# Optimization experiments

Hardware: AMD Instinct MI355X
Metric: run time of the kernel (lower is better)

## Reference

```python
import jax, jax.numpy as jnp
import numpy as np

H = 150  # hidden per direction

def _lstm_dir(x, w_ih, w_hh, b_ih, b_hh):
    # x: [B, T, D] -> hs: [B, T, H]; PyTorch gate order i,f,g,o
    B = x.shape[0]
    xg = jnp.einsum('btd,gd->btg', x, w_ih) + b_ih + b_hh  # precompute input projection [B,T,4H]
    def step(carry, xt):
        h, c = carry
        g = xt + h @ w_hh.T
        i, f, gg, o = jnp.split(g, 4, axis=-1)
        i, f, o = jax.nn.sigmoid(i), jax.nn.sigmoid(f), jax.nn.sigmoid(o)
        c = f * c + i * jnp.tanh(gg)
        h = o * jnp.tanh(c)
        return (h, c), h
    init = (jnp.zeros((B, H), x.dtype), jnp.zeros((B, H), x.dtype))
    _, hs = jax.lax.scan(step, init, jnp.swapaxes(xg, 0, 1))  # [T,B,H]
    return jnp.swapaxes(hs, 0, 1)

def _bilstm(x, w_ih_f, w_hh_f, b_ih_f, b_hh_f, w_ih_b, w_hh_b, b_ih_b, b_hh_b):
    fwd = _lstm_dir(x, w_ih_f, w_hh_f, b_ih_f, b_hh_f)
    bwd = jnp.flip(_lstm_dir(jnp.flip(x, axis=1), w_ih_b, w_hh_b, b_ih_b, b_hh_b), axis=1)
    return jnp.concatenate([fwd, bwd], axis=-1)  # [B, T, 2H]

def setup_inputs() -> dict:
    key = jax.random.key(0)
    ks = jax.random.split(key, 20)
    s = 0.05
    d = {
        'sentences': jax.random.normal(ks[0], (1024, 128, 343), jnp.float32),
        'w_ih_f1': jax.random.normal(ks[1], (600, 343)) * s,
        'w_hh_f1': jax.random.normal(ks[2], (600, 150)) * s,
        'b_ih_f1': jax.random.normal(ks[3], (600,)) * s,
        'b_hh_f1': jax.random.normal(ks[4], (600,)) * s,
        'w_ih_b1': jax.random.normal(ks[5], (600, 343)) * s,
        'w_hh_b1': jax.random.normal(ks[6], (600, 150)) * s,
        'b_ih_b1': jax.random.normal(ks[7], (600,)) * s,
        'b_hh_b1': jax.random.normal(ks[8], (600,)) * s,
        'w_ih_f2': jax.random.normal(ks[9], (600, 300)) * s,
        'w_hh_f2': jax.random.normal(ks[10], (600, 150)) * s,
        'b_ih_f2': jax.random.normal(ks[11], (600,)) * s,
        'b_hh_f2': jax.random.normal(ks[12], (600,)) * s,
        'w_ih_b2': jax.random.normal(ks[13], (600, 300)) * s,
        'w_hh_b2': jax.random.normal(ks[14], (600, 150)) * s,
        'b_ih_b2': jax.random.normal(ks[15], (600,)) * s,
        'b_hh_b2': jax.random.normal(ks[16], (600,)) * s,
        'w_out': jax.random.normal(ks[17], (7, 300)) * s,
        'b_out': jax.random.normal(ks[18], (7,)) * s,
    }
    return d

def reference(sentences, w_ih_f1, w_hh_f1, b_ih_f1, b_hh_f1, w_ih_b1, w_hh_b1, b_ih_b1, b_hh_b1,
              w_ih_f2, w_hh_f2, b_ih_f2, b_hh_f2, w_ih_b2, w_hh_b2, b_ih_b2, b_hh_b2, w_out, b_out):
    # Layer 1: per-sentence BiLSTM over words, batched instead of a python loop (dropout is eval-mode identity)
    word_out = _bilstm(sentences, w_ih_f1, w_hh_f1, b_ih_f1, b_hh_f1, w_ih_b1, w_hh_b1, b_ih_b1, b_hh_b1)  # [S,T,300]
    sent_emb = jnp.max(word_out, axis=1)  # max-pool over words -> [S,300]
    # Layer 2: BiLSTM over the sequence of sentence embeddings (batch of 1 paragraph)
    sent_out = _bilstm(sent_emb[None], w_ih_f2, w_hh_f2, b_ih_f2, b_hh_f2, w_ih_b2, w_hh_b2, b_ih_b2, b_hh_b2)[0]  # [S,300]
    log_probs = jax.nn.log_softmax(sent_out @ w_out.T + b_out, axis=-1)  # [S,7]
    return log_probs
```

## Files before the change

kernel.cpp:

```cpp
#include <hip/hip_runtime.h>
#include <hip/hip_bf16.h>
#include <hip/hip_fp16.h>

typedef short bf16x8 __attribute__((ext_vector_type(8)));
typedef float f32x4 __attribute__((ext_vector_type(4)));
typedef unsigned short u16x4 __attribute__((ext_vector_type(4)));
typedef unsigned int uint32;

#define MFMA_B16(a,b,c) __builtin_amdgcn_mfma_f32_16x16x32_bf16(a,b,c,0,0,0)

#define NS   1024
#define TLEN 128
#define DD   343
#define HH   150
#define GG   600
#define KX   352
#define XR   360
#define HR   168
#define KXP  44
#define NP   640
#define NG2  640

#define OFF_WXP  0u
#define OFF_WHP  901120u
#define OFF_B1   1310720u
#define OFF_W2B  1315840u
#define OFF_W2I  1725440u
#define OFF_SE   3184640u
#define OFF_XG2  4413440u
#define OFF_H2O  9656320u
#define OFF_XG1  10885120ull

#define PE0 450560
#define PE1 655360
#define PE2 656640
#define PE3 861440
#define PE4 1226240

__device__ __forceinline__ float rcp_fast(float x) { return __builtin_amdgcn_rcpf(x); }
__device__ __forceinline__ float sigm(float x) { return rcp_fast(1.f + __expf(-x)); }
__device__ __forceinline__ float tanh_fast(float x) { return 1.f - 2.f * rcp_fast(__expf(2.f * x) + 1.f); }

__device__ __forceinline__ void bar_lds() {
  asm volatile("s_waitcnt lgkmcnt(0)" ::: "memory");
  __builtin_amdgcn_s_barrier();
  asm volatile("" ::: "memory");
}

__device__ __forceinline__ unsigned short f2bu(float v) {
  __hip_bfloat16 b = __float2bfloat16(v);
  return __builtin_bit_cast(unsigned short, b);
}

__global__ __launch_bounds__(256) void prep_kernel(
    const float* __restrict__ wif1, const float* __restrict__ whf1,
    const float* __restrict__ bif1, const float* __restrict__ bhf1,
    const float* __restrict__ wib1, const float* __restrict__ whb1,
    const float* __restrict__ bib1, const float* __restrict__ bhb1,
    const float* __restrict__ wif2, const float* __restrict__ wib2,
    const float* __restrict__ whf2, const float* __restrict__ whb2,
    __hip_bfloat16* __restrict__ WXp, __hip_bfloat16* __restrict__ WHp,
    float* __restrict__ B1, __hip_bfloat16* __restrict__ W2B, float* __restrict__ W2I)
{
  int i = blockIdx.x * 256 + threadIdx.x;
  if (i < PE0) {
    int d = i / 225280; int r = i - d * 225280;
    int p = r / 5120;   int r2 = r - p * 5120;
    int n2 = r2 >> 3;   int jj = r2 & 7;
    int k = p * 8 + jj;
    int g = n2 / 160, j = n2 - g * 160;
    const float* w = d ? wib1 : wif1;
    float v = (j < HH && k < DD) ? w[(g * HH + j) * DD + k] : 0.f;
    WXp[i] = __float2bfloat16(v);
  } else if (i < PE1) {
    int ii = i - PE0;
    int d = ii / 102400; int r = ii - d * 102400;
    int p = r / 5120;    int r2 = r - p * 5120;
    int n2 = r2 >> 3;    int jj = r2 & 7;
    int k = p * 8 + jj;
    int g = n2 / 160, j = n2 - g * 160;
    const float* w = d ? whb1 : whf1;
    float v = (j < HH && k < HH) ? w[(g * HH + j) * HH + k] : 0.f;
    WHp[ii] = __float2bfloat16(v);
  } else if (i < PE2) {
    int ii = i - PE1;
    int d = ii / NP; int n2 = ii - d * NP;
    int g = n2 / 160, j = n2 - g * 160;
    float v = 0.f;
    if (j < HH) {
      int n = g * HH + j;
      v = d ? (bib1[n] + bhb1[n]) : (bif1[n] + bhf1[n]);
    }
    B1[ii] = v;
  } else if (i < PE3) {
    int ii = i - PE2;
    int d = ii / 102400; int r = ii - d * 102400;
    int n2 = r / 160;    int k = r - n2 * 160;
    int g = n2 / 160, j = n2 - g * 160;
    const float* w = d ? whb2 : whf2;
    float v = (j < HH && k < HH) ? w[(g * HH + j) * HH + k] : 0.f;
    W2B[ii] = __float2bfloat16(v);
  } else if (i < PE4) {
    int ii = i - PE3;
    int d = ii / 182400; int r = ii - d * 182400;
    int k = r / 608;     int n = r - k * 608;
    const float* w = d ? wib2 : wif2;
    float v = (n < GG) ? w[n * 300 + k] : 0.f;
    W2I[ii] = v;
  }
}

#define GA_SMEM (128u * 720u)

__global__ __launch_bounds__(512) void xg1_gemm(
    const float* __restrict__ x, const __hip_bfloat16* __restrict__ WXp,
    const float* __restrict__ B1, __hip_bfloat16* __restrict__ XG1,
    int sBase, int CS)
{
  extern __shared__ char smem[];
  __hip_bfloat16* xsA = (__hip_bfloat16*)smem;

  const int mtl = blockIdx.x;
  const int sg = sBase + mtl;

  const int tid = threadIdx.x;
  const int lane = tid & 63;
  const int wv = tid >> 6;
  const int wr = wv >> 2;
  const int wc = wv & 3;
  const int c16 = lane & 15;
  const int kgrp = lane >> 4;

  for (int g = tid; g < 11264; g += 512) {
    int row = g / 88;
    int c4 = (g - row * 88) * 4;
    const float* src = x + ((size_t)sg * TLEN + row) * DD + c4;
    float v0 = 0.f, v1 = 0.f, v2 = 0.f, v3 = 0.f;
    if (c4 + 3 < DD) { v0 = src[0]; v1 = src[1]; v2 = src[2]; v3 = src[3]; }
    else {
      if (c4 < DD)     v0 = src[0];
      if (c4 + 1 < DD) v1 = src[1];
      if (c4 + 2 < DD) v2 = src[2];
    }
    u16x4 o;
    o.x = f2bu(v0); o.y = f2bu(v1); o.z = f2bu(v2); o.w = f2bu(v3);
    *(u16x4*)(smem + row * 720 + c4 * 2) = o;
  }
  bar_lds();

  for (int dir = 0; dir < 2; ++dir) {
    const __hip_bfloat16* WXd = WXp + (size_t)dir * KXP * NP * 8;
    __hip_bfloat16* outd = XG1 + ((size_t)dir * CS + mtl) * TLEN * NG2;

    #pragma unroll
    for (int nh = 0; nh < 2; ++nh) {
      const int nbase = nh * 320 + wc * 80;
      f32x4 acc[4][5];
      #pragma unroll
      for (int mi = 0; mi < 4; ++mi)
        #pragma unroll
        for (int nf = 0; nf < 5; ++nf) acc[mi][nf] = (f32x4){0.f, 0.f, 0.f, 0.f};

      for (int kk = 0; kk < 11; ++kk) {
        bf16x8 a[4], b[5];
        #pragma unroll
        for (int mi = 0; mi < 4; ++mi)
          a[mi] = *reinterpret_cast<const bf16x8*>(
              xsA + (wr * 64 + mi * 16 + c16) * XR + kk * 32 + kgrp * 8);
        #pragma unroll
        for (int nf = 0; nf < 5; ++nf)
          b[nf] = *reinterpret_cast<const bf16x8*>(
              WXd + ((size_t)(kk * 4 + kgrp) * NP + nbase + nf * 16 + c16) * 8);
        #pragma unroll
        for (int mi = 0; mi < 4; ++mi)
          #pragma unroll
          for (int nf = 0; nf < 5; ++nf)
            acc[mi][nf] = MFMA_B16(a[mi], b[nf], acc[mi][nf]);
      }

      float bias[5];
      #pragma unroll
      for (int nf = 0; nf < 5; ++nf)
        bias[nf] = B1[dir * NP + nbase + nf * 16 + c16];

      #pragma unroll
      for (int mi = 0; mi < 4; ++mi)
        #pragma unroll
        for (int r = 0; r < 4; ++r) {
          int t = wr * 64 + mi * 16 + kgrp * 4 + r;
          __hip_bfloat16* row = outd + (size_t)t * NG2;
          #pragma unroll
          for (int nf = 0; nf < 5; ++nf)
            row[nbase + nf * 16 + c16] = __float2bfloat16(acc[mi][nf][r] + bias[nf]);
        }
    }
  }
}

__global__ __launch_bounds__(640) void lstm1_rec(
    const __hip_bfloat16* __restrict__ XG1, const __hip_bfloat16* __restrict__ WHp,
    float* __restrict__ SE, int sBase, int CS)
{
  __shared__ __hip_bfloat16 hs[16 * HR];

  const int tid = threadIdx.x;
  const int lane = tid & 63;
  const int wv = tid >> 6;
  const int dir = blockIdx.x & 1;
  const int grp = blockIdx.x >> 1;
  const int cls0 = grp * 8;
  const int s0g = sBase + cls0;
  const int c16 = lane & 15;
  const int kgrp = lane >> 4;
  const int j = wv * 16 + c16;

  for (int e = tid; e < 16 * HR; e += 640) hs[e] = __float2bfloat16(0.f);

  const __hip_bfloat16* WHd = WHp + (size_t)dir * 20 * NP * 8;
  bf16x8 whr[5][4];
  #pragma unroll
  for (int kh = 0; kh < 5; ++kh)
    #pragma unroll
    for (int g4 = 0; g4 < 4; ++g4) {
      whr[kh][g4] = *reinterpret_cast<const bf16x8*>(
          WHd + ((size_t)(kh * 4 + kgrp) * NP + g4 * 160 + j) * 8);
      asm volatile("" : "+v"(whr[kh][g4]));
    }

  float creg[4] = {0.f, 0.f, 0.f, 0.f};
  float mxr[4] = {-3e38f, -3e38f, -3e38f, -3e38f};

  const __hip_bfloat16* xgd = XG1 + (size_t)dir * CS * TLEN * NG2;
  const int sentb = cls0 + (kgrp & 1) * 4;
  const int par = kgrp >> 1;

  float xq[16], xqN[16];
  #pragma unroll
  for (int g4 = 0; g4 < 4; ++g4)
    #pragma unroll
    for (int r = 0; r < 4; ++r) {
      int tt = dir ? (127 - par) : par;
      xq[g4 * 4 + r] = __bfloat162float(
          xgd[((size_t)(sentb + r) * TLEN + tt) * NG2 + g4 * 160 + j]);
    }
  __syncthreads();

  for (int p = 0; p < 64; ++p) {
    f32x4 acc[4];
    #pragma unroll
    for (int g4 = 0; g4 < 4; ++g4) {
      acc[g4][0] = xq[g4 * 4 + 0]; acc[g4][1] = xq[g4 * 4 + 1];
      acc[g4][2] = xq[g4 * 4 + 2]; acc[g4][3] = xq[g4 * 4 + 3];
    }
    if (p < 63) {
      #pragma unroll
      for (int g4 = 0; g4 < 4; ++g4)
        #pragma unroll
        for (int r = 0; r < 4; ++r) {
          int tl = 2 * (p + 1) + par;
          int tt = dir ? (127 - tl) : tl;
          xqN[g4 * 4 + r] = __bfloat162float(
              xgd[((size_t)(sentb + r) * TLEN + tt) * NG2 + g4 * 160 + j]);
        }
    }
    #pragma unroll
    for (int kh = 0; kh < 5; ++kh) {
      bf16x8 ah = *reinterpret_cast<const bf16x8*>(hs + c16 * HR + kh * 32 + kgrp * 8);
      #pragma unroll
      for (int g4 = 0; g4 < 4; ++g4)
        acc[g4] = MFMA_B16(ah, whr[kh][g4], acc[g4]);
    }
    {
      const bool act = (kgrp < 2);
      #pragma unroll
      for (int r = 0; r < 4; ++r) {
        float iv = sigm(acc[0][r]);
        float fv = sigm(acc[1][r]);
        float gv = tanh_fast(acc[2][r]);
        float ov = sigm(acc[3][r]);
        float cin = __shfl_xor(creg[r], 32);
        float cn = fv * cin + iv * gv;
        float h = ov * tanh_fast(cn);
        creg[r] = act ? cn : creg[r];
        mxr[r] = act ? fmaxf(mxr[r], h) : mxr[r];
        if (act) hs[(8 + kgrp * 4 + r) * HR + j] = __float2bfloat16(h);
      }
    }
    bar_lds();
    #pragma unroll
    for (int kh = 0; kh < 5; ++kh) {
      bf16x8 ah = *reinterpret_cast<const bf16x8*>(hs + c16 * HR + kh * 32 + kgrp * 8);
      #pragma unroll
      for (int g4 = 0; g4 < 4; ++g4)
        acc[g4] = MFMA_B16(ah, whr[kh][g4], acc[g4]);
    }
    {
      const bool act = (kgrp >= 2);
      #pragma unroll
      for (int r = 0; r < 4; ++r) {
        float iv = sigm(acc[0][r]);
        float fv = sigm(acc[1][r]);
        float gv = tanh_fast(acc[2][r]);
        float ov = sigm(acc[3][r]);
        float cin = __shfl_xor(creg[r], 32);
        float cn = fv * cin + iv * gv;
        float h = ov * tanh_fast(cn);
        creg[r] = act ? cn : creg[r];
        mxr[r] = act ? fmaxf(mxr[r], h) : mxr[r];
        if (act) {
          int s = (kgrp - 2) * 4 + r;
          hs[s * HR + j] = __float2bfloat16(h);
          hs[(8 + s) * HR + j] = __float2bfloat16(0.f);
        }
      }
    }
    bar_lds();
    #pragma unroll
    for (int q = 0; q < 16; ++q) xq[q] = xqN[q];
  }

  #pragma unroll
  for (int r = 0; r < 4; ++r) {
    float m = fmaxf(mxr[r], __shfl_xor(mxr[r], 32));
    if (kgrp < 2 && j < HH)
      SE[(size_t)(s0g + kgrp * 4 + r) * 300 + dir * HH + j] = m;
  }
}

__global__ __launch_bounds__(256, 1) void xg2_kernel(
    const float* __restrict__ SE, const float* __restrict__ W2I,
    const float* __restrict__ bif2, const float* __restrict__ bhf2,
    const float* __restrict__ bib2, const float* __restrict__ bhb2,
    float* __restrict__ XG2)
{
  __shared__ float se[32 * 304];
  const int d = blockIdx.x >> 5, st = blockIdx.x & 31, sb = st * 32;
  const int tid = threadIdx.x;
  for (int e = tid; e < 32 * 300; e += 256) {
    int si = e / 300, k = e - si * 300;
    se[si * 304 + k] = SE[(size_t)(sb + si) * 300 + k];
  }
  __syncthreads();
  for (int pass = 0; pass < 3; ++pass) {
    int n = pass * 256 + tid;
    if (n < GG) {
      int n2 = (n / 150) * 160 + (n % 150);
      float bias = d ? (bib2[n] + bhb2[n]) : (bif2[n] + bhf2[n]);
      float acc[32];
      #pragma unroll
      for (int si = 0; si < 32; ++si) acc[si] = bias;
      const float* wcol = W2I + (size_t)d * 300 * 608 + n;
      for (int k = 0; k < 300; ++k) {
        float wvv = wcol[(size_t)k * 608];
        #pragma unroll
        for (int si = 0; si < 32; ++si) acc[si] += wvv * se[si * 304 + k];
      }
      #pragma unroll
      for (int si = 0; si < 32; ++si)
        XG2[((size_t)d * NS + sb + si) * NG2 + n2] = acc[si];
    }
  }
  for (int e = tid; e < 32 * 40; e += 256) {
    int si = e / 40, q = e - si * 40;
    int g = q / 10, jp = 150 + (q - g * 10);
    XG2[((size_t)d * NS + sb + si) * NG2 + g * 160 + jp] = 0.f;
  }
}

__global__ __launch_bounds__(640) void lstm2_kernel(
    const __hip_bfloat16* __restrict__ W2B, const float* __restrict__ XG2,
    float* __restrict__ H2O)
{
  const int dir = blockIdx.x;
  const int tid = threadIdx.x;
  const int lane = tid & 63;
  const int wv = tid >> 6;
  const int c16 = lane & 15;
  const int kg = lane >> 4;
  const int j = wv * 16 + c16;
  __shared__ __align__(16) __hip_bfloat16 hbuf[2][160];

  const f32x4 ZERO4 = {0.f, 0.f, 0.f, 0.f};

  const __hip_bfloat16* Wd = W2B + (size_t)dir * NP * 160;
  bf16x8 wf[5][4];
  #pragma unroll
  for (int kt = 0; kt < 5; ++kt)
    #pragma unroll
    for (int g4 = 0; g4 < 4; ++g4) {
      wf[kt][g4] = *reinterpret_cast<const bf16x8*>(
          Wd + (size_t)(g4 * 160 + j) * 160 + kt * 32 + kg * 8);
      asm volatile("" : "+v"(wf[kt][g4]));
    }

  if (tid < 160) hbuf[0][tid] = __float2bfloat16(0.f);
  __syncthreads();

  float creg = 0.f;
  const float* xg = XG2 + (size_t)dir * NS * NG2;

  float xqC[8], xqN[8];
  #pragma unroll
  for (int q = 0; q < 2; ++q)
    #pragma unroll
    for (int g4 = 0; g4 < 4; ++g4) {
      int ss2 = dir ? (1023 - q) : q;
      xqC[q * 4 + g4] = xg[(size_t)ss2 * NG2 + g4 * 160 + j];
    }

  for (int grp = 0; grp < 512; ++grp) {
    #pragma unroll
    for (int q = 0; q < 2; ++q)
      #pragma unroll
      for (int g4 = 0; g4 < 4; ++g4) {
        int sl = grp * 2 + 2 + q;
        if (sl < 1024) {
          int ss2 = dir ? (1023 - sl) : sl;
          xqN[q * 4 + g4] = xg[(size_t)ss2 * NG2 + g4 * 160 + j];
        } else {
          xqN[q * 4 + g4] = 0.f;
        }
      }
    #pragma unroll
    for (int q = 0; q < 2; ++q) {
      const int step = grp * 2 + q;
      const int ss = dir ? (1023 - step) : step;
      bf16x8 hf[5];
      #pragma unroll
      for (int kt = 0; kt < 5; ++kt)
        hf[kt] = *reinterpret_cast<const bf16x8*>(&hbuf[q][kt * 32 + kg * 8]);
      f32x4 aA[4], aB[4];
      #pragma unroll
      for (int g4 = 0; g4 < 4; ++g4) {
        aA[g4] = MFMA_B16(hf[0], wf[0][g4], ZERO4);
        aB[g4] = MFMA_B16(hf[1], wf[1][g4], ZERO4);
      }
      #pragma unroll
      for (int g4 = 0; g4 < 4; ++g4) {
        aA[g4] = MFMA_B16(hf[2], wf[2][g4], aA[g4]);
        aB[g4] = MFMA_B16(hf[3], wf[3][g4], aB[g4]);
        aA[g4] = MFMA_B16(hf[4], wf[4][g4], aA[g4]);
      }
      float iv = sigm(aA[0][0] + aB[0][0] + xqC[q * 4 + 0]);
      float fv = sigm(aA[1][0] + aB[1][0] + xqC[q * 4 + 1]);
      float gv = tanh_fast(aA[2][0] + aB[2][0] + xqC[q * 4 + 2]);
      float ov = sigm(aA[3][0] + aB[3][0] + xqC[q * 4 + 3]);
      creg = fv * creg + iv * gv;
      float nh = ov * tanh_fast(creg);
      if (kg == 0) {
        hbuf[q ^ 1][j] = __float2bfloat16(nh);
        if (j < HH) H2O[(size_t)ss * 300 + dir * HH + j] = nh;
      }
      bar_lds();
    }
    #pragma unroll
    for (int q = 0; q < 8; ++q) xqC[q] = xqN[q];
  }
}

__global__ __launch_bounds__(256, 1) void head_kernel(
    const float* __restrict__ H2O, const float* __restrict__ w_out,
    const float* __restrict__ b_out, float* __restrict__ out)
{
  int s = blockIdx.x * 256 + threadIdx.x;
  if (s >= NS) return;
  float acc[7];
  #pragma unroll
  for (int c = 0; c < 7; ++c) acc[c] = b_out[c];
  const float* hrow = H2O + (size_t)s * 300;
  for (int k = 0; k < 300; ++k) {
    float hv = hrow[k];
    #pragma unroll
    for (int c = 0; c < 7; ++c) acc[c] += hv * w_out[c * 300 + k];
  }
  float m = acc[0];
  #pragma unroll
  for (int c = 1; c < 7; ++c) m = fmaxf(m, acc[c]);
  float sum = 0.f;
  #pragma unroll
  for (int c = 0; c < 7; ++c) sum += __expf(acc[c] - m);
  float lse = m + __logf(sum);
  #pragma unroll
  for (int c = 0; c < 7; ++c) out[s * 7 + c] = acc[c] - lse;
}

extern "C" void kernel_launch(void* const* d_in, const int* in_sizes, int n_in,
                              void* d_out, int out_size, void* d_ws, size_t ws_size,
                              hipStream_t stream) {
  const float* x      = (const float*)d_in[0];
  const float* wif1   = (const float*)d_in[1];
  const float* whf1   = (const float*)d_in[2];
  const float* bif1   = (const float*)d_in[3];
  const float* bhf1   = (const float*)d_in[4];
  const float* wib1   = (const float*)d_in[5];
  const float* whb1   = (const float*)d_in[6];
  const float* bib1   = (const float*)d_in[7];
  const float* bhb1   = (const float*)d_in[8];
  const float* wif2   = (const float*)d_in[9];
  const float* whf2   = (const float*)d_in[10];
  const float* bif2   = (const float*)d_in[11];
  const float* bhf2   = (const float*)d_in[12];
  const float* wib2   = (const float*)d_in[13];
  const float* whb2   = (const float*)d_in[14];
  const float* bib2   = (const float*)d_in[15];
  const float* bhb2   = (const float*)d_in[16];
  const float* w_out  = (const float*)d_in[17];
  const float* b_out  = (const float*)d_in[18];

  char* ws = (char*)d_ws;
  __hip_bfloat16* WXp = (__hip_bfloat16*)(ws + OFF_WXP);
  __hip_bfloat16* WHp = (__hip_bfloat16*)(ws + OFF_WHP);
  float*    B1  = (float*)(ws + OFF_B1);
  __hip_bfloat16* W2B = (__hip_bfloat16*)(ws + OFF_W2B);
  float*    W2I = (float*)(ws + OFF_W2I);
  float*    SE  = (float*)(ws + OFF_SE);
  float*    XG2 = (float*)(ws + OFF_XG2);
  float*    H2O = (float*)(ws + OFF_H2O);
  __hip_bfloat16* XG1 = (__hip_bfloat16*)(ws + OFF_XG1);

  int CS = 128;
  if (ws_size > OFF_XG1) {
    size_t avail = ws_size - OFF_XG1;
    CS = 1024;
    while (CS > 128 && (size_t)CS * 327680ull > avail) CS >>= 1;
  }

  prep_kernel<<<(PE4 + 255) / 256, 256, 0, stream>>>(
      wif1, whf1, bif1, bhf1, wib1, whb1, bib1, bhb1,
      wif2, wib2, whf2, whb2, WXp, WHp, B1, W2B, W2I);

  (void)hipFuncSetAttribute((const void*)xg1_gemm,
                            hipFuncAttributeMaxDynamicSharedMemorySize, GA_SMEM);
  for (int sBase = 0; sBase < NS; sBase += CS) {
    xg1_gemm<<<CS, 512, GA_SMEM, stream>>>(x, WXp, B1, XG1, sBase, CS);
    lstm1_rec<<<CS / 4, 640, 0, stream>>>(XG1, WHp, SE, sBase, CS);
  }

  xg2_kernel<<<64, 256, 0, stream>>>(SE, W2I, bif2, bhf2, bib2, bhb2, XG2);

  lstm2_kernel<<<2, 640, 0, stream>>>(W2B, XG2, H2O);

  head_kernel<<<4, 256, 0, stream>>>(H2O, w_out, b_out, (float*)d_out);
}
```

Measured before the change: 1.352 ms.

## Split xg1 GEMM blocks by time halves and parallelize lstm2 MFMA chains

The input-projection GEMM now launches two blocks per sentence, each handling 64 of the 128 timesteps. This halves shared memory and accumulator registers per block and doubles the block count, which should raise occupancy. The cost is that each block streams the full weight tile from global memory, so weight reads double. Separately, the lstm2 recurrence replaces two dependent MFMA accumulation chains per gate with five independent MFMAs summed in scalar registers, shortening the serial dependency on the latency-bound step.

```diff
diff --git a/kernel.cpp b/kernel.cpp
--- a/kernel.cpp
+++ b/kernel.cpp
@@ -110,7 +110,7 @@
   }
 }
 
-#define GA_SMEM (128u * 720u)
+#define GA_SMEM (64u * 720u)
 
 __global__ __launch_bounds__(512) void xg1_gemm(
     const float* __restrict__ x, const __hip_bfloat16* __restrict__ WXp,
@@ -120,7 +120,9 @@
   extern __shared__ char smem[];
   __hip_bfloat16* xsA = (__hip_bfloat16*)smem;
 
-  const int mtl = blockIdx.x;
+  const int bid = blockIdx.x;
+  const int mh = bid & 1;
+  const int mtl = bid >> 1;
   const int sg = sBase + mtl;
 
   const int tid = threadIdx.x;
@@ -131,10 +133,10 @@
   const int c16 = lane & 15;
   const int kgrp = lane >> 4;
 
-  for (int g = tid; g < 11264; g += 512) {
+  for (int g = tid; g < 5632; g += 512) {
     int row = g / 88;
     int c4 = (g - row * 88) * 4;
-    const float* src = x + ((size_t)sg * TLEN + row) * DD + c4;
+    const float* src = x + (((size_t)sg * TLEN + mh * 64 + row)) * DD + c4;
     float v0 = 0.f, v1 = 0.f, v2 = 0.f, v3 = 0.f;
     if (c4 + 3 < DD) { v0 = src[0]; v1 = src[1]; v2 = src[2]; v3 = src[3]; }
     else {
@@ -155,24 +157,24 @@
     #pragma unroll
     for (int nh = 0; nh < 2; ++nh) {
       const int nbase = nh * 320 + wc * 80;
-      f32x4 acc[4][5];
-      #pragma unroll
-      for (int mi = 0; mi < 4; ++mi)
+      f32x4 acc[2][5];
+      #pragma unroll
+      for (int mi = 0; mi < 2; ++mi)
         #pragma unroll
         for (int nf = 0; nf < 5; ++nf) acc[mi][nf] = (f32x4){0.f, 0.f, 0.f, 0.f};
 
       for (int kk = 0; kk < 11; ++kk) {
-        bf16x8 a[4], b[5];
-        #pragma unroll
-        for (int mi = 0; mi < 4; ++mi)
+        bf16x8 a[2], b[5];
+        #pragma unroll
+        for (int mi = 0; mi < 2; ++mi)
           a[mi] = *reinterpret_cast<const bf16x8*>(
-              xsA + (wr * 64 + mi * 16 + c16) * XR + kk * 32 + kgrp * 8);
+              xsA + (wr * 32 + mi * 16 + c16) * XR + kk * 32 + kgrp * 8);
         #pragma unroll
         for (int nf = 0; nf < 5; ++nf)
           b[nf] = *reinterpret_cast<const bf16x8*>(
               WXd + ((size_t)(kk * 4 + kgrp) * NP + nbase + nf * 16 + c16) * 8);
         #pragma unroll
-        for (int mi = 0; mi < 4; ++mi)
+        for (int mi = 0; mi < 2; ++mi)
           #pragma unroll
           for (int nf = 0; nf < 5; ++nf)
             acc[mi][nf] = MFMA_B16(a[mi], b[nf], acc[mi][nf]);
@@ -184,10 +186,10 @@
         bias[nf] = B1[dir * NP + nbase + nf * 16 + c16];
 
       #pragma unroll
-      for (int mi = 0; mi < 4; ++mi)
+      for (int mi = 0; mi < 2; ++mi)
         #pragma unroll
         for (int r = 0; r < 4; ++r) {
-          int t = wr * 64 + mi * 16 + kgrp * 4 + r;
+          int t = mh * 64 + wr * 32 + mi * 16 + kgrp * 4 + r;
           __hip_bfloat16* row = outd + (size_t)t * NG2;
           #pragma unroll
           for (int nf = 0; nf < 5; ++nf)
@@ -429,22 +431,20 @@
       #pragma unroll
       for (int kt = 0; kt < 5; ++kt)
         hf[kt] = *reinterpret_cast<const bf16x8*>(&hbuf[q][kt * 32 + kg * 8]);
-      f32x4 aA[4], aB[4];
+      float y[4];
       #pragma unroll
       for (int g4 = 0; g4 < 4; ++g4) {
-        aA[g4] = MFMA_B16(hf[0], wf[0][g4], ZERO4);
-        aB[g4] = MFMA_B16(hf[1], wf[1][g4], ZERO4);
-      }
-      #pragma unroll
-      for (int g4 = 0; g4 < 4; ++g4) {
-        aA[g4] = MFMA_B16(hf[2], wf[2][g4], aA[g4]);
-        aB[g4] = MFMA_B16(hf[3], wf[3][g4], aB[g4]);
-        aA[g4] = MFMA_B16(hf[4], wf[4][g4], aA[g4]);
-      }
-      float iv = sigm(aA[0][0] + aB[0][0] + xqC[q * 4 + 0]);
-      float fv = sigm(aA[1][0] + aB[1][0] + xqC[q * 4 + 1]);
-      float gv = tanh_fast(aA[2][0] + aB[2][0] + xqC[q * 4 + 2]);
-      float ov = sigm(aA[3][0] + aB[3][0] + xqC[q * 4 + 3]);
+        f32x4 c0 = MFMA_B16(hf[0], wf[0][g4], ZERO4);
+        f32x4 c1 = MFMA_B16(hf[1], wf[1][g4], ZERO4);
+        f32x4 c2 = MFMA_B16(hf[2], wf[2][g4], ZERO4);
+        f32x4 c3 = MFMA_B16(hf[3], wf[3][g4], ZERO4);
+        f32x4 c4 = MFMA_B16(hf[4], wf[4][g4], ZERO4);
+        y[g4] = ((c0[0] + c1[0]) + (c2[0] + c3[0])) + c4[0];
+      }
+      float iv = sigm(y[0] + xqC[q * 4 + 0]);
+      float fv = sigm(y[1] + xqC[q * 4 + 1]);
+      float gv = tanh_fast(y[2] + xqC[q * 4 + 2]);
+      float ov = sigm(y[3] + xqC[q * 4 + 3]);
       creg = fv * creg + iv * gv;
       float nh = ov * tanh_fast(creg);
       if (kg == 0) {
@@ -532,7 +532,7 @@
   (void)hipFuncSetAttribute((const void*)xg1_gemm,
                             hipFuncAttributeMaxDynamicSharedMemorySize, GA_SMEM);
   for (int sBase = 0; sBase < NS; sBase += CS) {
-    xg1_gemm<<<CS, 512, GA_SMEM, stream>>>(x, WXp, B1, XG1, sBase, CS);
+    xg1_gemm<<<2 * CS, 512, GA_SMEM, stream>>>(x, WXp, B1, XG1, sBase, CS);
     lstm1_rec<<<CS / 4, 640, 0, stream>>>(XG1, WHp, SE, sBase, CS);
   }
 
```

New measurement: 1.692 ms. 1.25x slower.
